# Kernel optimization log

Measured on AMD Instinct MI355X. Metric: run time of the kernel, lower is better.

## Reference

```python
import jax, jax.numpy as jnp
import numpy as np

HIDDEN = 64
GROUPS = 512
GROUP_SIZE = 256  # all groups equal-sized and contiguous in ind_id
N = GROUPS * GROUP_SIZE
NEG_SLOPE = 0.1


def setup_inputs() -> dict:
    key = jax.random.key(0)
    k1, k2, k3 = jax.random.split(key, 3)
    h = jax.random.normal(k1, (N, HIDDEN), dtype=jnp.float32)
    # contiguous equal groups: ind_id = [0,0,...,0,1,1,...]
    ind_id = jnp.repeat(jnp.arange(GROUPS, dtype=jnp.int32), GROUP_SIZE)
    # torch.nn.Linear weights: W.weight [H, H], att.weight [1, 2H+1]
    W = jax.random.normal(k2, (HIDDEN, HIDDEN), dtype=jnp.float32) / np.sqrt(HIDDEN)
    att_w = jax.random.normal(k3, (2 * HIDDEN + 1,), dtype=jnp.float32) / np.sqrt(2 * HIDDEN + 1)
    return {"h": h, "ind_id": ind_id, "W": W, "att_w": att_w}


def reference(h, ind_id, W, att_w):
    # Wh = Linear(h); torch Linear: x @ W.T
    Wh = h @ W.T                                   # [N, H]
    a_src = att_w[:HIDDEN]                         # multiplies Wh_i (row index)
    a_dst = att_w[HIDDEN:2 * HIDDEN]               # multiplies Wh_j (col index)
    a_e = att_w[2 * HIDDEN]                        # multiplies the constant e_ij = 1
    s = Wh @ a_src                                 # [N]
    t = Wh @ a_dst                                 # [N]
    # ind_id is contiguous equal groups -> reshape to [G, M, ...]
    Whg = Wh.reshape(GROUPS, GROUP_SIZE, HIDDEN)
    sg = s.reshape(GROUPS, GROUP_SIZE)
    tg = t.reshape(GROUPS, GROUP_SIZE)
    # e[g,i,j] = leaky_relu(a_src.Wh[i] + a_dst.Wh[j] + a_e)
    e = jax.nn.leaky_relu(sg[:, :, None] + tg[:, None, :] + a_e,
                          negative_slope=NEG_SLOPE)  # [G, M, M]
    alpha = jax.nn.softmax(e, axis=-1)             # softmax over j (torch dim=1)
    out = jnp.einsum('gij,gjh->gih', alpha, Whg)   # [G, M, H]
    return out.reshape(N, HIDDEN)
```

## Files before the change

kernel.cpp:

```cpp
#include <hip/hip_runtime.h>
#include <math.h>

#define NEG_SLOPE 0.1f
#define LOG2E 1.4426950408889634f
#define GROUPS 512

typedef _Float16 half8  __attribute__((ext_vector_type(8)));
typedef _Float16 half4t __attribute__((ext_vector_type(4)));
typedef __fp16   pk16x2 __attribute__((ext_vector_type(2)));
typedef float    f32x4  __attribute__((ext_vector_type(4)));

__device__ __forceinline__ f32x4 mfma_f16(half8 a, half8 b, f32x4 c) {
    return __builtin_amdgcn_mfma_f32_16x16x32_f16(a, b, c, 0, 0, 0);
}

__global__ __launch_bounds__(1024)
void egat_fused(const float* __restrict__ Hin,
                const float* __restrict__ Wm,
                const float* __restrict__ att,
                float* __restrict__ Out)
{
    const int g    = blockIdx.x;
    const int tid  = threadIdx.x;
    const int w    = tid >> 6;
    const int lane = tid & 63;
    const int lg   = lane >> 4;
    const int lc   = lane & 15;

    __shared__ __align__(16) _Float16 fragV[8 * 4 * 64 * 8];
    __shared__ __align__(16) _Float16 WtF[2 * 4 * 64 * 8];
    __shared__ __align__(16) float u_lds[128];
    __shared__ __align__(16) float s_lds[256];
    __shared__ __align__(16) float t_lds[256];

    half8 Ahi[2], Alo[2];
    {
        const float* rp = Hin + (size_t)(g * 256 + w * 16 + lc) * 64 + lg * 8;
        #pragma unroll
        for (int kt = 0; kt < 2; ++kt) {
            f32x4 f0 = *(const f32x4*)(rp + kt * 32);
            f32x4 f1 = *(const f32x4*)(rp + kt * 32 + 4);
            half8 hi, lo;
            #pragma unroll
            for (int e = 0; e < 4; ++e) {
                _Float16 a0 = (_Float16)f0[e], a1 = (_Float16)f1[e];
                hi[e]     = a0;  lo[e]     = (_Float16)(f0[e] - (float)a0);
                hi[e + 4] = a1;  lo[e + 4] = (_Float16)(f1[e] - (float)a1);
            }
            Ahi[kt] = hi;
            Alo[kt] = lo;
        }
    }
    const float ae = att[128];

    if (w == 0) {
        float us = 0.f, ut = 0.f;
        #pragma unroll 16
        for (int o = 0; o < 64; ++o) {
            float wv = Wm[o * 64 + lane];
            us = fmaf(wv, att[o], us);
            ut = fmaf(wv, att[64 + o], ut);
        }
        u_lds[lane]      = us;
        u_lds[64 + lane] = ut;
    }

    if (tid < 512) {
        const int fr = tid;
        const int ln = fr & 63;
        const int ot = (fr >> 6) & 3;
        const int kt = fr >> 8;
        const float* wp = Wm + (ot * 16 + (ln & 15)) * 64 + kt * 32 + (ln >> 4) * 8;
        half8 hi;
        #pragma unroll
        for (int e = 0; e < 8; ++e) hi[e] = (_Float16)wp[e];
        *(half8*)&WtF[fr * 8] = hi;
    }
    __syncthreads();

    half8 Shi[2], Slo[2];
    #pragma unroll
    for (int kt = 0; kt < 2; ++kt) {
        if (lc < 2) {
            const float* up = &u_lds[lc * 64 + kt * 32 + lg * 8];
            f32x4 a = *(const f32x4*)up;
            f32x4 b2 = *(const f32x4*)(up + 4);
            #pragma unroll
            for (int e = 0; e < 4; ++e) {
                _Float16 h0 = (_Float16)a[e], h1 = (_Float16)b2[e];
                Shi[kt][e]     = h0;  Slo[kt][e]     = (_Float16)(a[e] - (float)h0);
                Shi[kt][e + 4] = h1;  Slo[kt][e + 4] = (_Float16)(b2[e] - (float)h1);
            }
        } else {
            #pragma unroll
            for (int e = 0; e < 8; ++e) { Shi[kt][e] = (_Float16)0.f; Slo[kt][e] = (_Float16)0.f; }
        }
    }

    f32x4 acc[5];
    #pragma unroll
    for (int ot = 0; ot < 5; ++ot) acc[ot] = f32x4{0.f, 0.f, 0.f, 0.f};

    #pragma unroll
    for (int kt = 0; kt < 2; ++kt) {
        #pragma unroll
        for (int ot = 0; ot < 4; ++ot) {
            half8 bh = *(half8*)&WtF[((kt * 4 + ot) * 64 + lane) * 8];
            acc[ot] = mfma_f16(Ahi[kt], bh, acc[ot]);
        }
        acc[4] = mfma_f16(Ahi[kt], Shi[kt], acc[4]);
        acc[4] = mfma_f16(Ahi[kt], Slo[kt], acc[4]);
        acc[4] = mfma_f16(Alo[kt], Shi[kt], acc[4]);
    }

    #pragma unroll
    for (int r = 0; r < 4; ++r) {
        int row = w * 16 + lg * 4 + r;
        float v = acc[4][r];
        if (lc == 0)      s_lds[row] = (v + ae) * LOG2E;
        else if (lc == 1) t_lds[row] = v * LOG2E;
    }

    {
        const int ktv   = w >> 1;
        const int lane2 = (2 * (w & 1) + (lg >> 1)) * 16 + lc;
        const int eb    = (lg & 1) * 4;
        #pragma unroll
        for (int ot = 0; ot < 4; ++ot) {
            half4t v;
            #pragma unroll
            for (int r = 0; r < 4; ++r) v[r] = (_Float16)acc[ot][r];
            *(half4t*)&fragV[((ktv * 4 + ot) * 64 + lane2) * 8 + eb] = v;
        }
    }
    __syncthreads();

    const float sa = s_lds[w * 16 + lc];

    half8 ones;
    #pragma unroll
    for (int e = 0; e < 8; ++e) ones[e] = (_Float16)1.f;

    f32x4 acc2[5];
    #pragma unroll
    for (int ot = 0; ot < 5; ++ot) acc2[ot] = f32x4{0.f, 0.f, 0.f, 0.f};

    for (int ktv = 0; ktv < 8; ++ktv) {
        f32x4 t0 = *(const f32x4*)&t_lds[ktv * 32 + lg * 8];
        f32x4 t1 = *(const f32x4*)&t_lds[ktv * 32 + lg * 8 + 4];

        float p[8];
        #pragma unroll
        for (int e = 0; e < 8; ++e) {
            float z = sa + (e < 4 ? t0[e] : t1[e - 4]);
            float x = fmaxf(z, NEG_SLOPE * z);
            p[e] = __builtin_amdgcn_exp2f(x);
        }
        union { pk16x2 h2[4]; half8 h8; } pk;
        #pragma unroll
        for (int e = 0; e < 4; ++e)
            pk.h2[e] = __builtin_amdgcn_cvt_pkrtz(p[2 * e], p[2 * e + 1]);

        acc2[4] = mfma_f16(pk.h8, ones, acc2[4]);
        #pragma unroll
        for (int ot = 0; ot < 4; ++ot) {
            half8 bfr = *(half8*)&fragV[((ktv * 4 + ot) * 64 + lane) * 8];
            acc2[ot] = mfma_f16(pk.h8, bfr, acc2[ot]);
        }
    }

    const size_t orow0 = (size_t)(g * 256 + w * 16) * 64;
    #pragma unroll
    for (int r = 0; r < 4; ++r) {
        float inv = __builtin_amdgcn_rcpf(acc2[4][r]);
        float* op = Out + orow0 + (size_t)(lg * 4 + r) * 64 + lc;
        #pragma unroll
        for (int ot = 0; ot < 4; ++ot)
            op[ot * 16] = acc2[ot][r] * inv;
    }
}

extern "C" void kernel_launch(void* const* d_in, const int* in_sizes, int n_in,
                              void* d_out, int out_size, void* d_ws, size_t ws_size,
                              hipStream_t stream) {
    const float* h   = (const float*)d_in[0];
    const float* W   = (const float*)d_in[2];
    const float* att = (const float*)d_in[3];
    float* out = (float*)d_out;
    egat_fused<<<dim3(GROUPS), dim3(1024), 0, stream>>>(h, W, att, out);
}
```

Baseline: 25.52 us.

## Process two groups per block and prefetch both groups' inputs upfront

Each block now handles two groups in sequence, launching half as many blocks. The per-block setup (folding W with the attention vector and converting W into fragments) is amortized over two groups. Both groups' h rows are loaded into registers at the start so the second group's global load overlaps the first group's compute. The cost is more registers and LDS per block and fewer blocks (256) than the device's CUs, which can leave compute units idle and serialize the two groups' work within one block.

```diff
diff --git a/kernel.cpp b/kernel.cpp
--- a/kernel.cpp
+++ b/kernel.cpp
@@ -20,35 +20,27 @@
                 const float* __restrict__ att,
                 float* __restrict__ Out)
 {
-    const int g    = blockIdx.x;
     const int tid  = threadIdx.x;
     const int w    = tid >> 6;
     const int lane = tid & 63;
     const int lg   = lane >> 4;
     const int lc   = lane & 15;
-
-    __shared__ __align__(16) _Float16 fragV[8 * 4 * 64 * 8];
+    const int g0   = blockIdx.x * 2;
+
+    __shared__ __align__(16) _Float16 fragV[2][8 * 4 * 64 * 8];
     __shared__ __align__(16) _Float16 WtF[2 * 4 * 64 * 8];
     __shared__ __align__(16) float u_lds[128];
-    __shared__ __align__(16) float s_lds[256];
-    __shared__ __align__(16) float t_lds[256];
-
-    half8 Ahi[2], Alo[2];
-    {
-        const float* rp = Hin + (size_t)(g * 256 + w * 16 + lc) * 64 + lg * 8;
+    __shared__ __align__(16) float s_lds[2][256];
+    __shared__ __align__(16) float t_lds[2][256];
+
+    f32x4 hraw[2][4];
+    #pragma unroll
+    for (int p = 0; p < 2; ++p) {
+        const float* rp = Hin + (size_t)((g0 + p) * 256 + w * 16 + lc) * 64 + lg * 8;
         #pragma unroll
         for (int kt = 0; kt < 2; ++kt) {
-            f32x4 f0 = *(const f32x4*)(rp + kt * 32);
-            f32x4 f1 = *(const f32x4*)(rp + kt * 32 + 4);
-            half8 hi, lo;
-            #pragma unroll
-            for (int e = 0; e < 4; ++e) {
-                _Float16 a0 = (_Float16)f0[e], a1 = (_Float16)f1[e];
-                hi[e]     = a0;  lo[e]     = (_Float16)(f0[e] - (float)a0);
-                hi[e + 4] = a1;  lo[e + 4] = (_Float16)(f1[e] - (float)a1);
-            }
-            Ahi[kt] = hi;
-            Alo[kt] = lo;
+            hraw[p][kt * 2]     = *(const f32x4*)(rp + kt * 32);
+            hraw[p][kt * 2 + 1] = *(const f32x4*)(rp + kt * 32 + 4);
         }
     }
     const float ae = att[128];
@@ -97,86 +89,103 @@
         }
     }
 
-    f32x4 acc[5];
-    #pragma unroll
-    for (int ot = 0; ot < 5; ++ot) acc[ot] = f32x4{0.f, 0.f, 0.f, 0.f};
-
-    #pragma unroll
-    for (int kt = 0; kt < 2; ++kt) {
-        #pragma unroll
-        for (int ot = 0; ot < 4; ++ot) {
-            half8 bh = *(half8*)&WtF[((kt * 4 + ot) * 64 + lane) * 8];
-            acc[ot] = mfma_f16(Ahi[kt], bh, acc[ot]);
-        }
-        acc[4] = mfma_f16(Ahi[kt], Shi[kt], acc[4]);
-        acc[4] = mfma_f16(Ahi[kt], Slo[kt], acc[4]);
-        acc[4] = mfma_f16(Alo[kt], Shi[kt], acc[4]);
-    }
-
-    #pragma unroll
-    for (int r = 0; r < 4; ++r) {
-        int row = w * 16 + lg * 4 + r;
-        float v = acc[4][r];
-        if (lc == 0)      s_lds[row] = (v + ae) * LOG2E;
-        else if (lc == 1) t_lds[row] = v * LOG2E;
-    }
-
-    {
-        const int ktv   = w >> 1;
-        const int lane2 = (2 * (w & 1) + (lg >> 1)) * 16 + lc;
-        const int eb    = (lg & 1) * 4;
-        #pragma unroll
-        for (int ot = 0; ot < 4; ++ot) {
-            half4t v;
-            #pragma unroll
-            for (int r = 0; r < 4; ++r) v[r] = (_Float16)acc[ot][r];
-            *(half4t*)&fragV[((ktv * 4 + ot) * 64 + lane2) * 8 + eb] = v;
-        }
-    }
-    __syncthreads();
-
-    const float sa = s_lds[w * 16 + lc];
-
     half8 ones;
     #pragma unroll
     for (int e = 0; e < 8; ++e) ones[e] = (_Float16)1.f;
 
-    f32x4 acc2[5];
-    #pragma unroll
-    for (int ot = 0; ot < 5; ++ot) acc2[ot] = f32x4{0.f, 0.f, 0.f, 0.f};
-
-    for (int ktv = 0; ktv < 8; ++ktv) {
-        f32x4 t0 = *(const f32x4*)&t_lds[ktv * 32 + lg * 8];
-        f32x4 t1 = *(const f32x4*)&t_lds[ktv * 32 + lg * 8 + 4];
-
-        float p[8];
-        #pragma unroll
-        for (int e = 0; e < 8; ++e) {
-            float z = sa + (e < 4 ? t0[e] : t1[e - 4]);
-            float x = fmaxf(z, NEG_SLOPE * z);
-            p[e] = __builtin_amdgcn_exp2f(x);
-        }
-        union { pk16x2 h2[4]; half8 h8; } pk;
-        #pragma unroll
-        for (int e = 0; e < 4; ++e)
-            pk.h2[e] = __builtin_amdgcn_cvt_pkrtz(p[2 * e], p[2 * e + 1]);
-
-        acc2[4] = mfma_f16(pk.h8, ones, acc2[4]);
-        #pragma unroll
-        for (int ot = 0; ot < 4; ++ot) {
-            half8 bfr = *(half8*)&fragV[((ktv * 4 + ot) * 64 + lane) * 8];
-            acc2[ot] = mfma_f16(pk.h8, bfr, acc2[ot]);
-        }
-    }
-
-    const size_t orow0 = (size_t)(g * 256 + w * 16) * 64;
-    #pragma unroll
-    for (int r = 0; r < 4; ++r) {
-        float inv = __builtin_amdgcn_rcpf(acc2[4][r]);
-        float* op = Out + orow0 + (size_t)(lg * 4 + r) * 64 + lc;
-        #pragma unroll
-        for (int ot = 0; ot < 4; ++ot)
-            op[ot * 16] = acc2[ot][r] * inv;
+    #pragma unroll
+    for (int p = 0; p < 2; ++p) {
+        half8 Ahi[2], Alo[2];
+        #pragma unroll
+        for (int kt = 0; kt < 2; ++kt) {
+            f32x4 f0 = hraw[p][kt * 2], f1 = hraw[p][kt * 2 + 1];
+            half8 hi, lo;
+            #pragma unroll
+            for (int e = 0; e < 4; ++e) {
+                _Float16 a0 = (_Float16)f0[e], a1 = (_Float16)f1[e];
+                hi[e]     = a0;  lo[e]     = (_Float16)(f0[e] - (float)a0);
+                hi[e + 4] = a1;  lo[e + 4] = (_Float16)(f1[e] - (float)a1);
+            }
+            Ahi[kt] = hi;
+            Alo[kt] = lo;
+        }
+
+        f32x4 acc[5];
+        #pragma unroll
+        for (int ot = 0; ot < 5; ++ot) acc[ot] = f32x4{0.f, 0.f, 0.f, 0.f};
+        #pragma unroll
+        for (int kt = 0; kt < 2; ++kt) {
+            #pragma unroll
+            for (int ot = 0; ot < 4; ++ot) {
+                half8 bh = *(half8*)&WtF[((kt * 4 + ot) * 64 + lane) * 8];
+                acc[ot] = mfma_f16(Ahi[kt], bh, acc[ot]);
+            }
+            acc[4] = mfma_f16(Ahi[kt], Shi[kt], acc[4]);
+            acc[4] = mfma_f16(Ahi[kt], Slo[kt], acc[4]);
+            acc[4] = mfma_f16(Alo[kt], Shi[kt], acc[4]);
+        }
+
+        #pragma unroll
+        for (int r = 0; r < 4; ++r) {
+            int row = w * 16 + lg * 4 + r;
+            float v = acc[4][r];
+            if (lc == 0)      s_lds[p][row] = (v + ae) * LOG2E;
+            else if (lc == 1) t_lds[p][row] = v * LOG2E;
+        }
+
+        {
+            const int ktv   = w >> 1;
+            const int lane2 = (2 * (w & 1) + (lg >> 1)) * 16 + lc;
+            const int eb    = (lg & 1) * 4;
+            #pragma unroll
+            for (int ot = 0; ot < 4; ++ot) {
+                half4t v;
+                #pragma unroll
+                for (int r = 0; r < 4; ++r) v[r] = (_Float16)acc[ot][r];
+                *(half4t*)&fragV[p][((ktv * 4 + ot) * 64 + lane2) * 8 + eb] = v;
+            }
+        }
+        __syncthreads();
+
+        const float sa = s_lds[p][w * 16 + lc];
+
+        f32x4 acc2[5];
+        #pragma unroll
+        for (int ot = 0; ot < 5; ++ot) acc2[ot] = f32x4{0.f, 0.f, 0.f, 0.f};
+
+        for (int ktv = 0; ktv < 8; ++ktv) {
+            f32x4 t0 = *(const f32x4*)&t_lds[p][ktv * 32 + lg * 8];
+            f32x4 t1 = *(const f32x4*)&t_lds[p][ktv * 32 + lg * 8 + 4];
+
+            float pr[8];
+            #pragma unroll
+            for (int e = 0; e < 8; ++e) {
+                float z = sa + (e < 4 ? t0[e] : t1[e - 4]);
+                float x = fmaxf(z, NEG_SLOPE * z);
+                pr[e] = __builtin_amdgcn_exp2f(x);
+            }
+            union { pk16x2 h2[4]; half8 h8; } pk;
+            #pragma unroll
+            for (int e = 0; e < 4; ++e)
+                pk.h2[e] = __builtin_amdgcn_cvt_pkrtz(pr[2 * e], pr[2 * e + 1]);
+
+            acc2[4] = mfma_f16(pk.h8, ones, acc2[4]);
+            #pragma unroll
+            for (int ot = 0; ot < 4; ++ot) {
+                half8 bfr = *(half8*)&fragV[p][((ktv * 4 + ot) * 64 + lane) * 8];
+                acc2[ot] = mfma_f16(pk.h8, bfr, acc2[ot]);
+            }
+        }
+
+        const size_t orow0 = (size_t)((g0 + p) * 256 + w * 16) * 64;
+        #pragma unroll
+        for (int r = 0; r < 4; ++r) {
+            float inv = __builtin_amdgcn_rcpf(acc2[4][r]);
+            float* op = Out + orow0 + (size_t)(lg * 4 + r) * 64 + lc;
+            #pragma unroll
+            for (int ot = 0; ot < 4; ++ot)
+                op[ot * 16] = acc2[ot][r] * inv;
+        }
     }
 }
 
@@ -187,5 +196,5 @@
     const float* W   = (const float*)d_in[2];
     const float* att = (const float*)d_in[3];
     float* out = (float*)d_out;
-    egat_fused<<<dim3(GROUPS), dim3(1024), 0, stream>>>(h, W, att, out);
+    egat_fused<<<dim3(GROUPS / 2), dim3(1024), 0, stream>>>(h, W, att, out);
 }
```

After: 24.58 us. 3.7% less time.
